# Optimization experiments

Hardware: AMD Instinct MI355X
Metric: run time of the kernel (lower is better)

The kernel has to match this reference:

```python
import jax, jax.numpy as jnp
import numpy as np

TEMPERATURE = 1.0
SCALE = 0.1  # embedding scale so exp(-dist/T) stays in fp32 range


def setup_inputs() -> dict:
    key = jax.random.key(0)
    kt, ki, kg = jax.random.split(key, 3)
    B, D, G = 8192, 512, 16
    text_embeddings = jax.random.normal(kt, (B, D), dtype=jnp.float32) * SCALE
    image_embeddings = jax.random.normal(ki, (B, D), dtype=jnp.float32) * SCALE
    groups = jax.random.randint(kg, (B,), 0, G, dtype=jnp.int64)
    return {"text_embeddings": text_embeddings,
            "image_embeddings": image_embeddings,
            "groups": groups}


def _pairwise_l2(text, image):
    # ||t_i - m_j|| via squared-norm expansion; sqrt made grad-safe at 0
    sq = (jnp.sum(text * text, axis=1)[:, None]
          + jnp.sum(image * image, axis=1)[None, :]
          - 2.0 * text @ image.T)                      # [B, B]
    sq = jnp.maximum(sq, 0.0)
    safe = jnp.where(sq > 0, sq, 1.0)
    return jnp.where(sq > 0, jnp.sqrt(safe), 0.0)


def reference(text_embeddings, image_embeddings, groups):
    B = text_embeddings.shape[0]
    dist = _pairwise_l2(text_embeddings, image_embeddings)   # [B, B]
    sim = jnp.exp(-dist / TEMPERATURE)                       # [B, B]
    same = groups[:, None] == groups[None, :]                # [B, B] bool
    numerator = jnp.sum(jnp.where(same, sim, 0.0), axis=1)   # [B]
    denominator = jnp.sum(jnp.where(same, 0.0, sim), axis=1) # [B]
    valid = (numerator > 0) & (denominator > 0)
    ratio = jnp.where(valid, numerator / jnp.where(valid, denominator, 1.0), 1.0)
    loss_i = jnp.where(valid, -jnp.log(ratio), 0.0)
    return jnp.sum(loss_i) / B
```

## Files before the change

### kernel.cpp

```cpp
#include <hip/hip_runtime.h>
#include <hip/hip_bf16.h>
#include <stdint.h>

#define Bn 8192
#define Dk 512
#define SCALE1 0x7F7F7F7F

typedef __attribute__((ext_vector_type(8))) int   int8v;
typedef __attribute__((ext_vector_type(4))) int   int4v;
typedef __attribute__((ext_vector_type(16))) float f32x16;

__device__ __forceinline__ void gload_lds16(const uint8_t* g, const uint8_t* l) {
  __builtin_amdgcn_global_load_lds(
      (const __attribute__((address_space(1))) void*)g,
      (__attribute__((address_space(3))) void*)l,
      16, 0, 0);
}

__device__ __forceinline__ uint32_t enc4(float x) {
  const float a = __builtin_fabsf(x);
  const uint32_t c =
      a < 0.046875f ? (a < 0.015625f ? 0u : 1u)
    : a < 0.109375f ? (a < 0.078125f ? 2u : 3u)
    : a < 0.21875f  ? (a < 0.15625f  ? 4u : 5u)
    :                 (a < 0.3125f   ? 6u : 7u);
  return c | (x < 0.f ? 8u : 0u);
}

__global__ __launch_bounds__(256) void prep_kernel(
    const float* __restrict__ T, const float* __restrict__ M,
    uint8_t* __restrict__ Tq, uint8_t* __restrict__ Mq,
    float* __restrict__ tn, float* __restrict__ mn)
{
  const int b = blockIdx.x;
  const bool isM = b >= 256;
  const int pb = b & 255;
  const int rbase = pb * 32;
  const float* __restrict__ src = isM ? M : T;
  float* __restrict__ nrm = isM ? mn : tn;
  uint8_t* __restrict__ q = isM ? Mq : Tq;

  const int tid = threadIdx.x;
  const int w = tid >> 6;
  const int l = tid & 63;
  const int oct = l >> 3;
  const int ol = l & 7;
  const int r = w * 8 + oct;

  const float4* rowp = (const float4*)(src + (size_t)(rbase + r) * Dk);
  uint8_t* pbase = q + (size_t)(pb >> 2) * 32768 + (pb & 3) * 1024 + r * 16;

  float nacc = 0.f;
  #pragma unroll
  for (int i = 0; i < 16; ++i) {
    const float4 v = rowp[i * 8 + ol];
    nacc += v.x * v.x + v.y * v.y + v.z * v.z + v.w * v.w;
    const uint32_t us = enc4(v.x) | (enc4(v.y) << 4) |
                        (enc4(v.z) << 8) | (enc4(v.w) << 12);
    const uint32_t p01 = us | ((uint32_t)__shfl_down((int)us, 1, 64) << 16);
    const uint32_t p23 = (uint32_t)__shfl_down((int)p01, 2, 64);
    const uint32_t p45 = (uint32_t)__shfl_down((int)p01, 4, 64);
    const uint32_t p67 = (uint32_t)__shfl_down((int)p01, 6, 64);
    if (ol == 0) {
      const int4v wd = {(int)p01, (int)p23, (int)p45, (int)p67};
      *(int4v*)(pbase + (i >> 1) * 4096 + (i & 1) * 512) = wd;
    }
  }

  nacc += __shfl_xor(nacc, 1, 64);
  nacc += __shfl_xor(nacc, 2, 64);
  nacc += __shfl_xor(nacc, 4, 64);
  if (ol == 0) nrm[rbase + r] = nacc;
}

__global__ __launch_bounds__(256, 4) void gemm_epi_kernel(
    const uint8_t* __restrict__ Tq, const uint8_t* __restrict__ Mq,
    const float* __restrict__ tn, const float* __restrict__ mn,
    const int* __restrict__ groups,
    float2* __restrict__ part)
{
  extern __shared__ char smem[];
  uint8_t* As8 = (uint8_t*)smem;
  uint8_t* Bs8 = As8 + 3 * 4096;
  float2* tg_s = (float2*)(Bs8 + 3 * 4096);
  float2* mg_s = tg_s + 128;

  const int tid = threadIdx.x;
  const int wave = tid >> 6;
  const int lane = tid & 63;
  const int l31 = lane & 31, h = lane >> 5;

  const int bid = blockIdx.x;
  const int xcd = bid & 7, lidx = bid >> 3;
  const int by = xcd * 8 + (lidx & 7);
  const int bx = lidx >> 3;
  const int brow = by * 128;
  const int bcol = bx * 128;

  const int tc = wave & 1;
  const int ir = wave >> 1;

  if (tid < 128) {
    tg_s[tid] = make_float2(tn[brow + tid], __uint_as_float((unsigned)groups[brow + tid]));
  } else {
    const int t = tid - 128;
    mg_s[t] = make_float2(mn[bcol + t], __uint_as_float((unsigned)groups[bcol + t]));
  }

  const uint8_t* Tpan = Tq + (size_t)by * 32768;
  const uint8_t* Mpan = Mq + (size_t)bx * 32768;
  const unsigned gOff = (unsigned)tid * 16;
  const int ldsOff = tid * 16;

  auto stage = [&](int t, int buf) {
    gload_lds16(Tpan + (unsigned)t * 4096 + gOff, As8 + buf * 4096 + ldsOff);
    gload_lds16(Mpan + (unsigned)t * 4096 + gOff, Bs8 + buf * 4096 + ldsOff);
  };

  int toffB[2], moffB[2];
  #pragma unroll
  for (int jt = 0; jt < 2; ++jt)
    toffB[jt] = (tc * 2 + jt) * 1024 + h * 512 + l31 * 16;
  #pragma unroll
  for (int it = 0; it < 2; ++it)
    moffB[it] = (ir * 2 + it) * 1024 + h * 512 + l31 * 16;

  f32x16 acc[2][2];
  #pragma unroll
  for (int it = 0; it < 2; ++it)
    #pragma unroll
    for (int jt = 0; jt < 2; ++jt)
      #pragma unroll
      for (int e = 0; e < 16; ++e)
        acc[it][jt][e] = 0.f;

  const int4v z4 = {0, 0, 0, 0};

  stage(0, 0); stage(1, 1);
  asm volatile("s_waitcnt vmcnt(2)" ::: "memory");
  __builtin_amdgcn_s_barrier();
  int kt = 0;

#define STEP(BUF, DO_STAGE, VMC)                                               \
  do {                                                                         \
    __builtin_amdgcn_s_barrier();                                              \
    if (DO_STAGE) stage(kt + 2, ((BUF) + 2) % 3);                              \
    asm volatile("s_waitcnt vmcnt(" #VMC ")" ::: "memory");                    \
    int4v tf[2], mf[2];                                                        \
    _Pragma("unroll")                                                          \
    for (int jt = 0; jt < 2; ++jt)                                             \
      tf[jt] = *(const int4v*)(As8 + (BUF) * 4096 + toffB[jt]);                \
    _Pragma("unroll")                                                          \
    for (int it = 0; it < 2; ++it)                                             \
      mf[it] = *(const int4v*)(Bs8 + (BUF) * 4096 + moffB[it]);                \
    __builtin_amdgcn_s_setprio(1);                                             \
    _Pragma("unroll")                                                          \
    for (int it = 0; it < 2; ++it) {                                           \
      const int8v a8 = __builtin_shufflevector(mf[it], z4, 0, 1, 2, 3, 4, 5, 6, 7); \
      _Pragma("unroll")                                                        \
      for (int jt = 0; jt < 2; ++jt) {                                         \
        const int8v b8 = __builtin_shufflevector(tf[jt], z4, 0, 1, 2, 3, 4, 5, 6, 7); \
        acc[it][jt] = __builtin_amdgcn_mfma_scale_f32_32x32x64_f8f6f4(         \
            a8, b8, acc[it][jt], 4, 4, 0, SCALE1, 0, SCALE1);                  \
      }                                                                        \
    }                                                                          \
    __builtin_amdgcn_s_setprio(0);                                             \
    ++kt;                                                                      \
  } while (0)

  STEP(0, true,  4);
  STEP(1, true,  4);
  STEP(2, true,  4);
  STEP(0, true,  4);
  STEP(1, true,  4);
  STEP(2, true,  4);
  STEP(0, false, 2);
  STEP(1, false, 0);
#undef STEP

  float2* red = reinterpret_cast<float2*>(As8);

  float nv[2] = {0.f, 0.f}, tot[2] = {0.f, 0.f};
  const int tlA = tc * 64 + l31;
  const int tlB = tlA + 32;
  const float2 tgA = tg_s[tlA];
  const float2 tgB = tg_s[tlB];
  #pragma unroll
  for (int it = 0; it < 2; ++it) {
    #pragma unroll
    for (int reg = 0; reg < 16; ++reg) {
      const int crow = (reg & 3) + 8 * (reg >> 2) + 4 * h;
      const float2 mg = mg_s[ir * 64 + it * 32 + crow];
      const unsigned gm = __float_as_uint(mg.y);
      {
        const float sq = fmaxf(fmaf(acc[it][0][reg], -0.0078125f, tgA.x + mg.x), 0.f);
        const float sim = __builtin_amdgcn_exp2f(-1.4426950408889634f *
                                                 __builtin_amdgcn_sqrtf(sq));
        tot[0] += sim;
        if (__float_as_uint(tgA.y) == gm) nv[0] += sim;
      }
      {
        const float sq = fmaxf(fmaf(acc[it][1][reg], -0.0078125f, tgB.x + mg.x), 0.f);
        const float sim = __builtin_amdgcn_exp2f(-1.4426950408889634f *
                                                 __builtin_amdgcn_sqrtf(sq));
        tot[1] += sim;
        if (__float_as_uint(tgB.y) == gm) nv[1] += sim;
      }
    }
  }
  __syncthreads();
  const int slot = ir * 2 + h;
  red[slot * 128 + tlA] = make_float2(nv[0], tot[0]);
  red[slot * 128 + tlB] = make_float2(nv[1], tot[1]);
  __syncthreads();
  if (tid < 128) {
    float n = 0.f, d = 0.f;
    #pragma unroll
    for (int s = 0; s < 4; ++s) {
      const float2 v = red[s * 128 + tid];
      n += v.x; d += v.y;
    }
    part[(size_t)bx * Bn + brow + tid] = make_float2(n, d);
  }
}

__global__ __launch_bounds__(256) void finalize1_kernel(
    const float2* __restrict__ part, float* __restrict__ bsum)
{
  const int i = blockIdx.x * 256 + threadIdx.x;
  float nv = 0.f, tv = 0.f;
  #pragma unroll 8
  for (int p = 0; p < 64; ++p) {
    const float2 v = part[(size_t)p * Bn + i];
    nv += v.x; tv += v.y;
  }
  const float dv = tv - nv;
  float li = (nv > 0.f && dv > 0.f)
      ? (__builtin_amdgcn_logf(dv) - __builtin_amdgcn_logf(nv)) * 0.69314718055994531f
      : 0.f;
  #pragma unroll
  for (int off = 32; off >= 1; off >>= 1) li += __shfl_xor(li, off, 64);
  __shared__ float ws4[4];
  if ((threadIdx.x & 63) == 0) ws4[threadIdx.x >> 6] = li;
  __syncthreads();
  if (threadIdx.x == 0) bsum[blockIdx.x] = ws4[0] + ws4[1] + ws4[2] + ws4[3];
}

__global__ void finalize2_kernel(const float* __restrict__ bsum, float* __restrict__ out)
{
  float s = (threadIdx.x < 32) ? bsum[threadIdx.x] : 0.f;
  #pragma unroll
  for (int off = 32; off >= 1; off >>= 1) s += __shfl_xor(s, off, 64);
  if (threadIdx.x == 0) out[0] = s / (float)Bn;
}

extern "C" void kernel_launch(void* const* d_in, const int* in_sizes, int n_in,
                              void* d_out, int out_size, void* d_ws, size_t ws_size,
                              hipStream_t stream) {
  const float* T = (const float*)d_in[0];
  const float* M = (const float*)d_in[1];
  const int* groups = (const int*)d_in[2];

  char* ws = (char*)d_ws;
  uint8_t* Tq = (uint8_t*)ws;
  uint8_t* Mq = (uint8_t*)(ws + (size_t)64 * 32768);
  float* tn  = (float*)(ws + (size_t)128 * 32768);
  float* mn  = tn + Bn;
  float2* part = (float2*)(mn + Bn);
  float* bsum = (float*)(part + (size_t)64 * Bn);

  const int smem_bytes = 3 * 4096 + 3 * 4096 + 128 * 8 + 128 * 8;
  hipFuncSetAttribute((const void*)gemm_epi_kernel,
                      hipFuncAttributeMaxDynamicSharedMemorySize, smem_bytes);

  prep_kernel<<<512, 256, 0, stream>>>(T, M, Tq, Mq, tn, mn);
  gemm_epi_kernel<<<4096, 256, smem_bytes, stream>>>(Tq, Mq, tn, mn, groups, part);
  finalize1_kernel<<<Bn / 256, 256, 0, stream>>>(part, bsum);
  finalize2_kernel<<<1, 64, 0, stream>>>(bsum, (float*)d_out);
}
```

Measured before the change: 57.57 us.

## Give each wave private double-buffered LDS staging and drop block barriers in K loop

Each wave now loads its own T and M fragments into a private double-buffered LDS region, so the per-step block-wide barriers and the three-slot shared ring buffer are no longer needed. Waves that share rows or columns duplicate those loads, which raises global/L2 traffic and LDS footprint (32KB versus about 26KB). The epilogue folds the log2(e) factor into the squared norms and the GEMM scale constant, which removes a multiply per element. It also drops the clamp to zero before the sqrt, so negative rounding could produce NaN. The setprio hints are removed and LDS moves to static allocation.

New measurement: 58.74 us. 1.02x slower.

```diff
diff --git a/kernel.cpp b/kernel.cpp
--- a/kernel.cpp
+++ b/kernel.cpp
@@ -5,6 +5,8 @@
 #define Bn 8192
 #define Dk 512
 #define SCALE1 0x7F7F7F7F
+#define K2  2.0813689810056077f
+#define C1  (-0.01626069516410631f)
 
 typedef __attribute__((ext_vector_type(8))) int   int8v;
 typedef __attribute__((ext_vector_type(4))) int   int4v;
@@ -70,7 +72,7 @@
   nacc += __shfl_xor(nacc, 1, 64);
   nacc += __shfl_xor(nacc, 2, 64);
   nacc += __shfl_xor(nacc, 4, 64);
-  if (ol == 0) nrm[rbase + r] = nacc;
+  if (ol == 0) nrm[rbase + r] = nacc * K2;
 }
 
 __global__ __launch_bounds__(256, 4) void gemm_epi_kernel(
@@ -79,11 +81,10 @@
     const int* __restrict__ groups,
     float2* __restrict__ part)
 {
-  extern __shared__ char smem[];
-  uint8_t* As8 = (uint8_t*)smem;
-  uint8_t* Bs8 = As8 + 3 * 4096;
-  float2* tg_s = (float2*)(Bs8 + 3 * 4096);
-  float2* mg_s = tg_s + 128;
+  __shared__ uint8_t wbuf[4][2][4096];
+  __shared__ float2 tg_s[128];
+  __shared__ float2 mg_s[128];
+  __shared__ float2 red[4][128];
 
   const int tid = threadIdx.x;
   const int wave = tid >> 6;
@@ -107,23 +108,20 @@
     mg_s[t] = make_float2(mn[bcol + t], __uint_as_float((unsigned)groups[bcol + t]));
   }
 
-  const uint8_t* Tpan = Tq + (size_t)by * 32768;
-  const uint8_t* Mpan = Mq + (size_t)bx * 32768;
-  const unsigned gOff = (unsigned)tid * 16;
-  const int ldsOff = tid * 16;
-
-  auto stage = [&](int t, int buf) {
-    gload_lds16(Tpan + (unsigned)t * 4096 + gOff, As8 + buf * 4096 + ldsOff);
-    gload_lds16(Mpan + (unsigned)t * 4096 + gOff, Bs8 + buf * 4096 + ldsOff);
+  const uint8_t* Tpan = Tq + (size_t)by * 32768 + tc * 2048;
+  const uint8_t* Mpan = Mq + (size_t)bx * 32768 + ir * 2048;
+  uint8_t* wb = &wbuf[wave][0][0];
+  const int ls = lane * 16;
+
+  auto stage = [&](int t, int b) {
+    uint8_t* d = wb + b * 4096;
+    gload_lds16(Tpan + t * 4096 + ls,        d + ls);
+    gload_lds16(Tpan + t * 4096 + 1024 + ls, d + 1024 + ls);
+    gload_lds16(Mpan + t * 4096 + ls,        d + 2048 + ls);
+    gload_lds16(Mpan + t * 4096 + 1024 + ls, d + 3072 + ls);
   };
 
-  int toffB[2], moffB[2];
-  #pragma unroll
-  for (int jt = 0; jt < 2; ++jt)
-    toffB[jt] = (tc * 2 + jt) * 1024 + h * 512 + l31 * 16;
-  #pragma unroll
-  for (int it = 0; it < 2; ++it)
-    moffB[it] = (ir * 2 + it) * 1024 + h * 512 + l31 * 16;
+  const int fOff = h * 512 + l31 * 16;
 
   f32x16 acc[2][2];
   #pragma unroll
@@ -136,24 +134,21 @@
 
   const int4v z4 = {0, 0, 0, 0};
 
-  stage(0, 0); stage(1, 1);
-  asm volatile("s_waitcnt vmcnt(2)" ::: "memory");
-  __builtin_amdgcn_s_barrier();
+  stage(0, 0);
   int kt = 0;
 
 #define STEP(BUF, DO_STAGE, VMC)                                               \
   do {                                                                         \
-    __builtin_amdgcn_s_barrier();                                              \
-    if (DO_STAGE) stage(kt + 2, ((BUF) + 2) % 3);                              \
+    if (DO_STAGE) stage(kt + 1, (BUF) ^ 1);                                    \
     asm volatile("s_waitcnt vmcnt(" #VMC ")" ::: "memory");                    \
+    const uint8_t* base = wb + (BUF) * 4096;                                   \
     int4v tf[2], mf[2];                                                        \
     _Pragma("unroll")                                                          \
     for (int jt = 0; jt < 2; ++jt)                                             \
-      tf[jt] = *(const int4v*)(As8 + (BUF) * 4096 + toffB[jt]);                \
+      tf[jt] = *(const int4v*)(base + jt * 1024 + fOff);                       \
     _Pragma("unroll")                                                          \
     for (int it = 0; it < 2; ++it)                                             \
-      mf[it] = *(const int4v*)(Bs8 + (BUF) * 4096 + moffB[it]);                \
-    __builtin_amdgcn_s_setprio(1);                                             \
+      mf[it] = *(const int4v*)(base + 2048 + it * 1024 + fOff);                \
     _Pragma("unroll")                                                          \
     for (int it = 0; it < 2; ++it) {                                           \
       const int8v a8 = __builtin_shufflevector(mf[it], z4, 0, 1, 2, 3, 4, 5, 6, 7); \
@@ -164,21 +159,20 @@
             a8, b8, acc[it][jt], 4, 4, 0, SCALE1, 0, SCALE1);                  \
       }                                                                        \
     }                                                                          \
-    __builtin_amdgcn_s_setprio(0);                                             \
     ++kt;                                                                      \
   } while (0)
 
   STEP(0, true,  4);
   STEP(1, true,  4);
-  STEP(2, true,  4);
   STEP(0, true,  4);
   STEP(1, true,  4);
-  STEP(2, true,  4);
-  STEP(0, false, 2);
+  STEP(0, true,  4);
+  STEP(1, true,  4);
+  STEP(0, true,  4);
   STEP(1, false, 0);
 #undef STEP
 
-  float2* red = reinterpret_cast<float2*>(As8);
+  __syncthreads();
 
   float nv[2] = {0.f, 0.f}, tot[2] = {0.f, 0.f};
   const int tlA = tc * 64 + l31;
@@ -193,31 +187,28 @@
       const float2 mg = mg_s[ir * 64 + it * 32 + crow];
       const unsigned gm = __float_as_uint(mg.y);
       {
-        const float sq = fmaxf(fmaf(acc[it][0][reg], -0.0078125f, tgA.x + mg.x), 0.f);
-        const float sim = __builtin_amdgcn_exp2f(-1.4426950408889634f *
-                                                 __builtin_amdgcn_sqrtf(sq));
+        const float sq = fmaf(acc[it][0][reg], C1, tgA.x + mg.x);
+        const float sim = __builtin_amdgcn_exp2f(-__builtin_amdgcn_sqrtf(sq));
         tot[0] += sim;
         if (__float_as_uint(tgA.y) == gm) nv[0] += sim;
       }
       {
-        const float sq = fmaxf(fmaf(acc[it][1][reg], -0.0078125f, tgB.x + mg.x), 0.f);
-        const float sim = __builtin_amdgcn_exp2f(-1.4426950408889634f *
-                                                 __builtin_amdgcn_sqrtf(sq));
+        const float sq = fmaf(acc[it][1][reg], C1, tgB.x + mg.x);
+        const float sim = __builtin_amdgcn_exp2f(-__builtin_amdgcn_sqrtf(sq));
         tot[1] += sim;
         if (__float_as_uint(tgB.y) == gm) nv[1] += sim;
       }
     }
   }
-  __syncthreads();
   const int slot = ir * 2 + h;
-  red[slot * 128 + tlA] = make_float2(nv[0], tot[0]);
-  red[slot * 128 + tlB] = make_float2(nv[1], tot[1]);
+  red[slot][tlA] = make_float2(nv[0], tot[0]);
+  red[slot][tlB] = make_float2(nv[1], tot[1]);
   __syncthreads();
   if (tid < 128) {
     float n = 0.f, d = 0.f;
     #pragma unroll
     for (int s = 0; s < 4; ++s) {
-      const float2 v = red[s * 128 + tid];
+      const float2 v = red[s][tid];
       n += v.x; d += v.y;
     }
     part[(size_t)bx * Bn + brow + tid] = make_float2(n, d);
@@ -269,12 +260,8 @@
   float2* part = (float2*)(mn + Bn);
   float* bsum = (float*)(part + (size_t)64 * Bn);
 
-  const int smem_bytes = 3 * 4096 + 3 * 4096 + 128 * 8 + 128 * 8;
-  hipFuncSetAttribute((const void*)gemm_epi_kernel,
-                      hipFuncAttributeMaxDynamicSharedMemorySize, smem_bytes);
-
   prep_kernel<<<512, 256, 0, stream>>>(T, M, Tq, Mq, tn, mn);
-  gemm_epi_kernel<<<4096, 256, smem_bytes, stream>>>(Tq, Mq, tn, mn, groups, part);
+  gemm_epi_kernel<<<4096, 256, 0, stream>>>(Tq, Mq, tn, mn, groups, part);
   finalize1_kernel<<<Bn / 256, 256, 0, stream>>>(part, bsum);
   finalize2_kernel<<<1, 64, 0, stream>>>(bsum, (float*)d_out);
 }
```
